# Kernel optimization log

Measured on AMD Instinct MI355X. Metric: run time of the kernel, lower is better.

## Reference

```python
import jax, jax.numpy as jnp
import numpy as np

D_MODEL = 2048
NUM_HEADS = 16
D_K = D_MODEL // NUM_HEADS


def setup_inputs() -> dict:
    key = jax.random.key(0)
    k_x, k_wqkv, k_bqkv, k_wo, k_bo = jax.random.split(key, 5)
    B, S = 2, 2048
    x = jax.random.normal(k_x, (B, S, D_MODEL), dtype=jnp.float32)
    # torch Linear init scale ~ 1/sqrt(fan_in); stored here as [in, out] for x @ W
    s = 1.0 / np.sqrt(D_MODEL)
    W_qkv = jax.random.uniform(k_wqkv, (D_MODEL, 3 * D_MODEL), minval=-s, maxval=s, dtype=jnp.float32)
    b_qkv = jax.random.uniform(k_bqkv, (3 * D_MODEL,), minval=-s, maxval=s, dtype=jnp.float32)
    W_out = jax.random.uniform(k_wo, (D_MODEL, D_MODEL), minval=-s, maxval=s, dtype=jnp.float32)
    b_out = jax.random.uniform(k_bo, (D_MODEL,), minval=-s, maxval=s, dtype=jnp.float32)
    return {"x": x, "W_qkv": W_qkv, "b_qkv": b_qkv, "W_out": W_out, "b_out": b_out}


def reference(x, W_qkv, b_qkv, W_out, b_out):
    B, S, D = x.shape
    qkv = x @ W_qkv + b_qkv                      # [B, S, 3*D]
    qkv = qkv.reshape(B, S, NUM_HEADS, 3 * D_K).transpose(0, 2, 1, 3)  # [B, H, S, 3*d_k]
    q, k, v = jnp.split(qkv, 3, axis=-1)          # each [B, H, S, d_k]
    scores = jnp.einsum("bhqd,bhkd->bhqk", q, k) / jnp.sqrt(jnp.float32(D_K))
    attn = jax.nn.softmax(scores, axis=-1)        # dropout is identity in eval mode
    out = jnp.einsum("bhqk,bhkd->bhqd", attn, v)  # [B, H, S, d_k]
    out = out.transpose(0, 2, 1, 3).reshape(B, S, D)
    return out @ W_out + b_out
```

## Files before the change

### kernel.cpp

```cpp
#include <hip/hip_runtime.h>
#include <hip/hip_bf16.h>

typedef unsigned short ushort_t;
typedef short short8 __attribute__((ext_vector_type(8)));
typedef short short4v __attribute__((ext_vector_type(4)));
typedef float floatx4 __attribute__((ext_vector_type(4)));

#define MFMA16(a,b,c) __builtin_amdgcn_mfma_f32_16x16x32_bf16((a),(b),(c),0,0,0)

#define D_MODEL 2048
#define NHEAD   16
#define DK      128
#define SEQ     2048
#define BATCH   2

static __device__ __forceinline__ ushort_t f2bf(float f){
  union { float f; unsigned int i; } v; v.f = f;
  unsigned int r = v.i + 0x7FFFu + ((v.i >> 16) & 1u);
  return (ushort_t)(r >> 16);
}

typedef __attribute__((address_space(3))) void       lds_void_t;
typedef __attribute__((address_space(1))) const void gbl_void_t;
#define GLOAD_LDS16(g, l) \
  __builtin_amdgcn_global_load_lds((gbl_void_t*)(g), (lds_void_t*)(l), 16, 0, 0)

__global__ __launch_bounds__(256) void cvt_k(const float* __restrict__ in,
                                             ushort_t* __restrict__ out) {
  int i = (blockIdx.x * 256 + threadIdx.x) * 8;
  floatx4 a = *(const floatx4*)&in[i];
  floatx4 b = *(const floatx4*)&in[i + 4];
  short8 r;
  for (int j = 0; j < 4; ++j) r[j] = (short)f2bf(a[j]);
  for (int j = 0; j < 4; ++j) r[4 + j] = (short)f2bf(b[j]);
  *(short8*)&out[i] = r;
}

__global__ __launch_bounds__(256) void transpose_cvt_k(const float* __restrict__ in,
                                                       ushort_t* __restrict__ out,
                                                       int R, int C) {
  __shared__ ushort_t tile[64][65];
  int tr = blockIdx.y * 64, tc = blockIdx.x * 64;
  int t = threadIdx.x;
  for (int p = 0; p < 16; ++p) {
    int idx = t + p * 256;
    int r = idx >> 6, c = idx & 63;
    tile[r][c] = f2bf(in[(size_t)(tr + r) * C + (tc + c)]);
  }
  __syncthreads();
  for (int p = 0; p < 16; ++p) {
    int idx = t + p * 256;
    int r = idx >> 6, c = idx & 63;
    out[(size_t)(tc + r) * R + (tr + c)] = tile[c][r];
  }
}

template <int MODE>
__global__ __launch_bounds__(256) void gemm_nt(const ushort_t* __restrict__ A,
                                               const ushort_t* __restrict__ BT,
                                               const float* __restrict__ bias,
                                               ushort_t* __restrict__ out_q,
                                               ushort_t* __restrict__ out_k,
                                               ushort_t* __restrict__ out_v,
                                               float* __restrict__ outp,
                                               int M, int N, int K) {
  __shared__ __align__(16) ushort_t As[128 * 32];
  __shared__ __align__(16) ushort_t Bs[128 * 32];
  const int bn = blockIdx.x, bm = blockIdx.y;
  const int t = threadIdx.x;
  const int wave = t >> 6, lane = t & 63;
  const int wr = (wave >> 1) * 64, wc = (wave & 1) * 64;
  const int l15 = lane & 15, lg = lane >> 4;
  const int row0 = bm * 128, col0 = bn * 128;

  floatx4 acc[4][4];
#pragma unroll
  for (int m = 0; m < 4; ++m)
#pragma unroll
    for (int n = 0; n < 4; ++n) acc[m][n] = (floatx4){0.f, 0.f, 0.f, 0.f};

  const int r_in = lane >> 2;
  const int c_in = (lane & 3) * 8;

  for (int k0 = 0; k0 < K; k0 += 32) {
#pragma unroll
    for (int t2 = 0; t2 < 2; ++t2) {
      int blkr = (wave * 2 + t2) * 16;
      GLOAD_LDS16(&A[(size_t)(row0 + blkr + r_in) * K + k0 + c_in], &As[blkr * 32]);
      GLOAD_LDS16(&BT[(size_t)(col0 + blkr + r_in) * K + k0 + c_in], &Bs[blkr * 32]);
    }
    __syncthreads();
    short8 af[4], bfr[4];
#pragma unroll
    for (int m = 0; m < 4; ++m) af[m]  = *(const short8*)&As[(wr + m * 16 + l15) * 32 + lg * 8];
#pragma unroll
    for (int n = 0; n < 4; ++n) bfr[n] = *(const short8*)&Bs[(wc + n * 16 + l15) * 32 + lg * 8];
#pragma unroll
    for (int m = 0; m < 4; ++m)
#pragma unroll
      for (int n = 0; n < 4; ++n)
        acc[m][n] = MFMA16(af[m], bfr[n], acc[m][n]);
    __syncthreads();
  }

  if (MODE == 1) {
#pragma unroll
    for (int m = 0; m < 4; ++m)
#pragma unroll
      for (int n = 0; n < 4; ++n) {
        int c = col0 + wc + n * 16 + l15;
        float bv = bias[c];
        int r0 = row0 + wr + m * 16 + lg * 4;
#pragma unroll
        for (int j = 0; j < 4; ++j)
          outp[(size_t)(r0 + j) * N + c] = acc[m][n][j] + bv;
      }
  } else {
    const int h = bn / 3, which = bn - h * 3;
#pragma unroll
    for (int m = 0; m < 4; ++m)
#pragma unroll
      for (int n = 0; n < 4; ++n) {
        int d = wc + n * 16 + l15;
        float bv = bias[col0 + d];
        int r0 = row0 + wr + m * 16 + lg * 4;
        int b = r0 >> 11;
        int s0 = r0 & 2047;
        if (which < 2) {
          ushort_t* dst = (which == 0) ? out_q : out_k;
          size_t base = ((size_t)(b * NHEAD + h) * SEQ) * DK;
#pragma unroll
          for (int j = 0; j < 4; ++j)
            dst[base + (size_t)(s0 + j) * DK + d] = f2bf(acc[m][n][j] + bv);
        } else {
          size_t base = ((size_t)(b * NHEAD + h) * DK + d) * SEQ + s0;
          short4v tmp;
#pragma unroll
          for (int j = 0; j < 4; ++j) tmp[j] = (short)f2bf(acc[m][n][j] + bv);
          *(short4v*)&out_v[base] = tmp;
        }
      }
  }
}

__global__ __launch_bounds__(256, 2) void attn_k(const ushort_t* __restrict__ qws,
                                                 const ushort_t* __restrict__ kws,
                                                 const ushort_t* __restrict__ vtws,
                                                 ushort_t* __restrict__ ctx) {
  __shared__ __align__(16) ushort_t Ks[2][64 * 128];
  __shared__ __align__(16) ushort_t Vs[2][128 * 64];
  __shared__ __align__(16) ushort_t P[4][32 * 64];

  const int bid = blockIdx.y * gridDim.x + blockIdx.x;
  const int xcd = bid & 7, slot = bid >> 3;
  const int bh = xcd * 4 + (slot & 3);
  const int qt = slot >> 2;
  const int b = bh >> 4, h = bh & 15;
  const int t = threadIdx.x, wave = t >> 6, lane = t & 63;
  const int l15 = lane & 15, lg = lane >> 4;

  const ushort_t* Q  = qws  + (size_t)bh * SEQ * DK;
  const ushort_t* Kp = kws  + (size_t)bh * SEQ * DK;
  const ushort_t* VT = vtws + (size_t)bh * DK * SEQ;

  const int qr = qt * 128 + wave * 32;

  short8 qf[2][4];
#pragma unroll
  for (int m = 0; m < 2; ++m)
#pragma unroll
    for (int kk = 0; kk < 4; ++kk)
      qf[m][kk] = *(const short8*)&Q[(size_t)(qr + m * 16 + l15) * DK + kk * 32 + lg * 8];

  floatx4 o[2][8];
#pragma unroll
  for (int m = 0; m < 2; ++m)
#pragma unroll
    for (int n = 0; n < 8; ++n) o[m][n] = (floatx4){0.f, 0.f, 0.f, 0.f};
  float mrow[2] = {-1e30f, -1e30f};
  float lrowp[2] = {0.f, 0.f};

  char* Pb = (char*)&P[wave][0];
  const int swz = (l15 & 7) << 4;
  const float scale = 0.08838834764831845f;

  auto STAGE = [&](int buf, int kv0) {
#pragma unroll
    for (int t2 = 0; t2 < 4; ++t2) {
      int rowK = wave * 16 + t2 * 4 + (lane >> 4);
      int csK = ((lane & 15) * 16) ^ ((rowK & 7) << 4);
      GLOAD_LDS16((const char*)&Kp[(size_t)(kv0 + rowK) * DK] + csK,
                  (char*)&Ks[buf][0] + wave * 4096 + t2 * 1024);
      int rowV = wave * 32 + t2 * 8 + (lane >> 3);
      int csV = ((lane & 7) * 16) ^ ((rowV & 7) << 4);
      GLOAD_LDS16((const char*)&VT[(size_t)rowV * SEQ + kv0] + csV,
                  (char*)&Vs[buf][0] + wave * 4096 + t2 * 1024);
    }
  };

  STAGE(0, 0);
  __syncthreads();

  for (int it = 0; it < SEQ / 64; ++it) {
    const char* KsC = (const char*)&Ks[it & 1][0];
    const char* VsC = (const char*)&Vs[it & 1][0];
    if (it < SEQ / 64 - 1) STAGE((it + 1) & 1, (it + 1) * 64);

    floatx4 s[2][4];
#pragma unroll
    for (int m = 0; m < 2; ++m)
#pragma unroll
      for (int c = 0; c < 4; ++c) s[m][c] = (floatx4){0.f, 0.f, 0.f, 0.f};
#pragma unroll
    for (int c = 0; c < 4; ++c) {
      short8 kf[4];
#pragma unroll
      for (int kk = 0; kk < 4; ++kk)
        kf[kk] = *(const short8*)(KsC + (c * 16 + l15) * 256 + ((kk * 64 + lg * 16) ^ swz));
#pragma unroll
      for (int m = 0; m < 2; ++m)
#pragma unroll
        for (int kk = 0; kk < 4; ++kk)
          s[m][c] = MFMA16(kf[kk], qf[m][kk], s[m][c]);
    }

#pragma unroll
    for (int m = 0; m < 2; ++m) {
      float tt[4][4];
      float rm = -1e30f;
#pragma unroll
      for (int c = 0; c < 4; ++c)
#pragma unroll
        for (int j = 0; j < 4; ++j) {
          tt[c][j] = s[m][c][j] * scale;
          rm = fmaxf(rm, tt[c][j]);
        }
      rm = fmaxf(rm, __shfl_xor(rm, 16));
      rm = fmaxf(rm, __shfl_xor(rm, 32));

      if (__any(rm > mrow[m] + 8.f)) {
        float rmn = fmaxf(rm, mrow[m]);
        float corr = __expf(mrow[m] - rmn);
        mrow[m] = rmn;
        lrowp[m] *= corr;
        float co[4];
#pragma unroll
        for (int j = 0; j < 4; ++j) co[j] = __shfl(corr, lg * 4 + j);
#pragma unroll
        for (int n = 0; n < 8; ++n)
#pragma unroll
          for (int j = 0; j < 4; ++j) o[m][n][j] *= co[j];
      }

      float psum = 0.f;
#pragma unroll
      for (int c = 0; c < 4; ++c) {
        float p0 = __expf(tt[c][0] - mrow[m]);
        float p1 = __expf(tt[c][1] - mrow[m]);
        float p2 = __expf(tt[c][2] - mrow[m]);
        float p3 = __expf(tt[c][3] - mrow[m]);
        psum += (p0 + p1) + (p2 + p3);
        short4v pk;
        pk[0] = (short)f2bf(p0); pk[1] = (short)f2bf(p1);
        pk[2] = (short)f2bf(p2); pk[3] = (short)f2bf(p3);
        *(short4v*)(Pb + (m * 16 + l15) * 128 + ((c * 32 + lg * 8) ^ swz)) = pk;
      }
      lrowp[m] += psum;
    }

    asm volatile("s_waitcnt lgkmcnt(0)" ::: "memory");
    __builtin_amdgcn_sched_barrier(0);

    short8 pa[2][2];
#pragma unroll
    for (int m = 0; m < 2; ++m)
#pragma unroll
      for (int ch = 0; ch < 2; ++ch)
        pa[m][ch] = *(const short8*)(Pb + (m * 16 + l15) * 128 + ((ch * 64 + lg * 16) ^ swz));
#pragma unroll
    for (int n = 0; n < 8; ++n) {
      short8 v0 = *(const short8*)(VsC + (n * 16 + l15) * 128 + ((lg * 16) ^ swz));
      short8 v1 = *(const short8*)(VsC + (n * 16 + l15) * 128 + ((64 + lg * 16) ^ swz));
#pragma unroll
      for (int m = 0; m < 2; ++m) {
        o[m][n] = MFMA16(pa[m][0], v0, o[m][n]);
        o[m][n] = MFMA16(pa[m][1], v1, o[m][n]);
      }
    }
    __syncthreads();
  }

#pragma unroll
  for (int m = 0; m < 2; ++m) {
    lrowp[m] += __shfl_xor(lrowp[m], 16);
    lrowp[m] += __shfl_xor(lrowp[m], 32);
  }
#pragma unroll
  for (int m = 0; m < 2; ++m) {
    float rcp[4];
#pragma unroll
    for (int j = 0; j < 4; ++j) rcp[j] = 1.f / __shfl(lrowp[m], lg * 4 + j);
#pragma unroll
    for (int n = 0; n < 8; ++n)
#pragma unroll
      for (int j = 0; j < 4; ++j) {
        int row = qr + m * 16 + lg * 4 + j;
        ctx[(size_t)(b * SEQ + row) * D_MODEL + h * DK + n * 16 + l15] =
            f2bf(o[m][n][j] * rcp[j]);
      }
  }
}

extern "C" void kernel_launch(void* const* d_in, const int* in_sizes, int n_in,
                              void* d_out, int out_size, void* d_ws, size_t ws_size,
                              hipStream_t stream) {
  const float* x    = (const float*)d_in[0];
  const float* Wqkv = (const float*)d_in[1];
  const float* bqkv = (const float*)d_in[2];
  const float* Wout = (const float*)d_in[3];
  const float* bout = (const float*)d_in[4];
  float* out = (float*)d_out;

  ushort_t* WqkvT = (ushort_t*)d_ws;
  ushort_t* WoutT = WqkvT + (size_t)6144 * 2048;
  ushort_t* qws   = WoutT + (size_t)2048 * 2048;
  ushort_t* kws   = qws + (size_t)8388608;
  ushort_t* vtws  = kws + (size_t)8388608;
  ushort_t* ctx   = vtws + (size_t)8388608;
  ushort_t* xb    = ctx + (size_t)8388608;

  cvt_k<<<4096, 256, 0, stream>>>(x, xb);
  transpose_cvt_k<<<dim3(6144 / 64, 2048 / 64), 256, 0, stream>>>(Wqkv, WqkvT, 2048, 6144);
  transpose_cvt_k<<<dim3(2048 / 64, 2048 / 64), 256, 0, stream>>>(Wout, WoutT, 2048, 2048);

  gemm_nt<0><<<dim3(48, 32), 256, 0, stream>>>(xb, WqkvT, bqkv, qws, kws, vtws, nullptr,
                                               4096, 6144, 2048);
  attn_k<<<dim3(16, 32), 256, 0, stream>>>(qws, kws, vtws, ctx);
  gemm_nt<1><<<dim3(16, 32), 256, 0, stream>>>(ctx, WoutT, bout, nullptr, nullptr, nullptr, out,
                                               4096, 2048, 2048);
}
```

Before: 417.3 us.

## Rewrite projection GEMMs with double-buffered 128x256 tiles, LDS swizzle, and XCD remap

Both projection GEMMs now use a new 512-thread kernel with 128x256 output tiles and K-step 64. The LDS tiles are double-buffered so global-to-LDS loads for the next K tile overlap the MFMA work on the current one. LDS reads use an XOR swizzle to avoid bank conflicts, workgroup IDs are remapped across the 8 XCDs for L2 locality, and s_setprio raises wave priority around the MFMA blocks. The kernel hardcodes K=2048 and uses more LDS per block, which limits occupancy to one block per CU.

```diff
diff --git a/kernel.cpp b/kernel.cpp
--- a/kernel.cpp
+++ b/kernel.cpp
@@ -56,22 +56,32 @@
 }
 
 template <int MODE>
-__global__ __launch_bounds__(256) void gemm_nt(const ushort_t* __restrict__ A,
-                                               const ushort_t* __restrict__ BT,
-                                               const float* __restrict__ bias,
-                                               ushort_t* __restrict__ out_q,
-                                               ushort_t* __restrict__ out_k,
-                                               ushort_t* __restrict__ out_v,
-                                               float* __restrict__ outp,
-                                               int M, int N, int K) {
-  __shared__ __align__(16) ushort_t As[128 * 32];
-  __shared__ __align__(16) ushort_t Bs[128 * 32];
-  const int bn = blockIdx.x, bm = blockIdx.y;
-  const int t = threadIdx.x;
-  const int wave = t >> 6, lane = t & 63;
-  const int wr = (wave >> 1) * 64, wc = (wave & 1) * 64;
+__global__ __launch_bounds__(512, 1) void gemm8p(const ushort_t* __restrict__ A,
+                                                 const ushort_t* __restrict__ BT,
+                                                 const float* __restrict__ bias,
+                                                 ushort_t* __restrict__ out_q,
+                                                 ushort_t* __restrict__ out_k,
+                                                 ushort_t* __restrict__ out_v,
+                                                 float* __restrict__ outp,
+                                                 int N, int nbn) {
+  __shared__ __align__(16) ushort_t As[2][128 * 64];
+  __shared__ __align__(16) ushort_t Bs[2][256 * 64];
+
+  const int nwg = gridDim.x;
+  const int orig = blockIdx.x;
+  const int wg = (orig & 7) * (nwg >> 3) + (orig >> 3);
+  const int bm = wg / nbn, bn = wg - bm * nbn;
+  const int row0 = bm * 128, col0 = bn * 256;
+
+  const int t = threadIdx.x, wave = t >> 6, lane = t & 63;
+  const int wm = wave >> 2, wn = wave & 3;
   const int l15 = lane & 15, lg = lane >> 4;
-  const int row0 = bm * 128, col0 = bn * 128;
+  const int swz = (l15 & 7) << 4;
+  const int csrc = ((lane & 7) * 16) ^ ((lane >> 3) << 4);
+  const int rsub = lane >> 3;
+
+  char* AsC = (char*)&As[0][0];
+  char* BsC = (char*)&Bs[0][0];
 
   floatx4 acc[4][4];
 #pragma unroll
@@ -79,51 +89,95 @@
 #pragma unroll
     for (int n = 0; n < 4; ++n) acc[m][n] = (floatx4){0.f, 0.f, 0.f, 0.f};
 
-  const int r_in = lane >> 2;
-  const int c_in = (lane & 3) * 8;
-
-  for (int k0 = 0; k0 < K; k0 += 32) {
-#pragma unroll
-    for (int t2 = 0; t2 < 2; ++t2) {
-      int blkr = (wave * 2 + t2) * 16;
-      GLOAD_LDS16(&A[(size_t)(row0 + blkr + r_in) * K + k0 + c_in], &As[blkr * 32]);
-      GLOAD_LDS16(&BT[(size_t)(col0 + blkr + r_in) * K + k0 + c_in], &Bs[blkr * 32]);
-    }
-    __syncthreads();
-    short8 af[4], bfr[4];
-#pragma unroll
-    for (int m = 0; m < 4; ++m) af[m]  = *(const short8*)&As[(wr + m * 16 + l15) * 32 + lg * 8];
-#pragma unroll
-    for (int n = 0; n < 4; ++n) bfr[n] = *(const short8*)&Bs[(wc + n * 16 + l15) * 32 + lg * 8];
+#define STAGE_A(buf, k0, j) \
+  GLOAD_LDS16((const char*)&A[(size_t)(row0 + (j) * 64 + wave * 8 + rsub) * 2048 + (k0)] + csrc, \
+              AsC + (buf) * 16384 + ((j) * 64 + wave * 8) * 128)
+#define STAGE_B(buf, k0, j) \
+  GLOAD_LDS16((const char*)&BT[(size_t)(col0 + (j) * 64 + wave * 8 + rsub) * 2048 + (k0)] + csrc, \
+              BsC + (buf) * 32768 + ((j) * 64 + wave * 8) * 128)
+
+  STAGE_A(0, 0, 0); STAGE_A(0, 0, 1);
+  STAGE_B(0, 0, 0); STAGE_B(0, 0, 1); STAGE_B(0, 0, 2); STAGE_B(0, 0, 3);
+  asm volatile("s_waitcnt vmcnt(0)" ::: "memory");
+  __builtin_amdgcn_s_barrier();
+
+  for (int kt = 0; kt < 32; ++kt) {
+    const int buf = kt & 1, nb = buf ^ 1;
+    const int nk0 = (kt + 1) * 64;
+    const char* Ab = AsC + buf * 16384;
+    const char* Bb = BsC + buf * 32768;
+    short8 a[4], b[4];
+
+#pragma unroll
+    for (int m = 0; m < 4; ++m)
+      a[m] = *(const short8*)(Ab + (wm * 64 + m * 16 + l15) * 128 + ((lg * 16) ^ swz));
+#pragma unroll
+    for (int n = 0; n < 4; ++n)
+      b[n] = *(const short8*)(Bb + (wn * 64 + n * 16 + l15) * 128 + ((lg * 16) ^ swz));
+    if (kt < 31) {
+      STAGE_A(nb, nk0, 0); STAGE_A(nb, nk0, 1);
+      STAGE_B(nb, nk0, 0); STAGE_B(nb, nk0, 1);
+    }
+    __builtin_amdgcn_s_barrier();
+    asm volatile("s_waitcnt lgkmcnt(0)" ::: "memory");
+    __builtin_amdgcn_sched_barrier(0);
+    __builtin_amdgcn_s_setprio(1);
 #pragma unroll
     for (int m = 0; m < 4; ++m)
 #pragma unroll
       for (int n = 0; n < 4; ++n)
-        acc[m][n] = MFMA16(af[m], bfr[n], acc[m][n]);
-    __syncthreads();
-  }
+        acc[m][n] = MFMA16(a[m], b[n], acc[m][n]);
+    __builtin_amdgcn_s_setprio(0);
+    __builtin_amdgcn_s_barrier();
+
+#pragma unroll
+    for (int m = 0; m < 4; ++m)
+      a[m] = *(const short8*)(Ab + (wm * 64 + m * 16 + l15) * 128 + ((64 + lg * 16) ^ swz));
+#pragma unroll
+    for (int n = 0; n < 4; ++n)
+      b[n] = *(const short8*)(Bb + (wn * 64 + n * 16 + l15) * 128 + ((64 + lg * 16) ^ swz));
+    if (kt < 31) {
+      STAGE_B(nb, nk0, 2); STAGE_B(nb, nk0, 3);
+    }
+    __builtin_amdgcn_s_barrier();
+    asm volatile("s_waitcnt lgkmcnt(0)" ::: "memory");
+    __builtin_amdgcn_sched_barrier(0);
+    __builtin_amdgcn_s_setprio(1);
+#pragma unroll
+    for (int m = 0; m < 4; ++m)
+#pragma unroll
+      for (int n = 0; n < 4; ++n)
+        acc[m][n] = MFMA16(a[m], b[n], acc[m][n]);
+    __builtin_amdgcn_s_setprio(0);
+    asm volatile("s_waitcnt vmcnt(0)" ::: "memory");
+    __builtin_amdgcn_s_barrier();
+  }
+#undef STAGE_A
+#undef STAGE_B
 
   if (MODE == 1) {
 #pragma unroll
     for (int m = 0; m < 4; ++m)
 #pragma unroll
       for (int n = 0; n < 4; ++n) {
-        int c = col0 + wc + n * 16 + l15;
+        int c = col0 + wn * 64 + n * 16 + l15;
         float bv = bias[c];
-        int r0 = row0 + wr + m * 16 + lg * 4;
+        int r0 = row0 + wm * 64 + m * 16 + lg * 4;
 #pragma unroll
         for (int j = 0; j < 4; ++j)
           outp[(size_t)(r0 + j) * N + c] = acc[m][n][j] + bv;
       }
   } else {
-    const int h = bn / 3, which = bn - h * 3;
 #pragma unroll
     for (int m = 0; m < 4; ++m)
 #pragma unroll
       for (int n = 0; n < 4; ++n) {
-        int d = wc + n * 16 + l15;
-        float bv = bias[col0 + d];
-        int r0 = row0 + wr + m * 16 + lg * 4;
+        int c = col0 + wn * 64 + n * 16 + l15;
+        float bv = bias[c];
+        int blk = c >> 7;
+        int h = blk / 3, which = blk - h * 3;
+        int d = c & 127;
+        int r0 = row0 + wm * 64 + m * 16 + lg * 4;
         int b = r0 >> 11;
         int s0 = r0 & 2047;
         if (which < 2) {
@@ -333,9 +387,7 @@
   transpose_cvt_k<<<dim3(6144 / 64, 2048 / 64), 256, 0, stream>>>(Wqkv, WqkvT, 2048, 6144);
   transpose_cvt_k<<<dim3(2048 / 64, 2048 / 64), 256, 0, stream>>>(Wout, WoutT, 2048, 2048);
 
-  gemm_nt<0><<<dim3(48, 32), 256, 0, stream>>>(xb, WqkvT, bqkv, qws, kws, vtws, nullptr,
-                                               4096, 6144, 2048);
+  gemm8p<0><<<768, 512, 0, stream>>>(xb, WqkvT, bqkv, qws, kws, vtws, nullptr, 6144, 24);
   attn_k<<<dim3(16, 32), 256, 0, stream>>>(qws, kws, vtws, ctx);
-  gemm_nt<1><<<dim3(16, 32), 256, 0, stream>>>(ctx, WoutT, bout, nullptr, nullptr, nullptr, out,
-                                               4096, 2048, 2048);
-}
+  gemm8p<1><<<256, 512, 0, stream>>>(ctx, WoutT, bout, nullptr, nullptr, nullptr, out, 2048, 8);
+}
```

Result: faster. 397.5 us (-4.7%).
